# Kernel optimization log

Measured on AMD Instinct MI355X. Metric: run time of the kernel, lower is better.

The kernel has to match this reference:

```python
import jax, jax.numpy as jnp
import numpy as np

WS = 5       # window_size
SHIFT = 2    # shift_size
NH = 3       # num_heads (hardcoded in module)
EPS = 1e-5   # LayerNorm eps (torch default)

B, H, W, C = 4, 400, 400, 48


def _window_partition(x, ws):
    b, h, w, c = x.shape
    x = x.reshape(b, h // ws, ws, w // ws, ws, c).transpose(0, 1, 3, 2, 4, 5)
    return x.reshape(-1, ws * ws, c)  # [B*nH*nW, ws*ws, C]


def _window_reverse(x, ws, h, w):
    bn = x.shape[0] // ((h // ws) * (w // ws))
    x = x.reshape(bn, h // ws, w // ws, ws, ws, -1).transpose(0, 1, 3, 2, 4, 5)
    return x.reshape(bn, h, w, -1)


def _qkv_branch(win, qkv_w, qkv_b, ln_g, ln_b):
    # Linear -> LayerNorm(last dim) -> Softmax over window-position axis (dim 1)
    y = win @ qkv_w + qkv_b                      # [B_, N, 3C]
    mu = jnp.mean(y, axis=-1, keepdims=True)
    var = jnp.mean((y - mu) ** 2, axis=-1, keepdims=True)
    y = (y - mu) * jax.lax.rsqrt(var + EPS) * ln_g + ln_b
    y = jax.nn.softmax(y, axis=1)                # nn.Softmax(1)
    b_, n, _ = y.shape
    y = y.reshape(b_, n, 3, NH, C // NH).transpose(2, 0, 3, 1, 4)  # [3, B_, h, N, d]
    return y[0], y[1], y[2]


def setup_inputs() -> dict:
    key = jax.random.key(0)
    ks = jax.random.split(key, 4)
    lr_patch = jax.random.normal(ks[0], (B, H, W, C), jnp.float32)
    ref_patch = jax.random.normal(ks[1], (B, H, W, C), jnp.float32)
    qkv_w = jax.random.normal(ks[2], (C, 3 * C), jnp.float32) * (1.0 / np.sqrt(C))
    qkv_b = jax.random.normal(ks[3], (3 * C,), jnp.float32) * 0.01
    ln_g = jnp.ones((3 * C,), jnp.float32)
    ln_b = jnp.zeros((3 * C,), jnp.float32)
    return {"lr_patch": lr_patch, "ref_patch": ref_patch, "qkv_w": qkv_w,
            "qkv_b": qkv_b, "ln_g": ln_g, "ln_b": ln_b}


def reference(lr_patch, ref_patch, qkv_w, qkv_b, ln_g, ln_b):
    # cyclic shift
    s_lr = jnp.roll(lr_patch, shift=(-SHIFT, -SHIFT), axis=(1, 2))
    s_ref = jnp.roll(ref_patch, shift=(-SHIFT, -SHIFT), axis=(1, 2))

    lr_w = _window_partition(s_lr, WS)    # [B_, N=25, C]
    ref_w = _window_partition(s_ref, WS)

    q_lr, k_lr, v_lr = _qkv_branch(lr_w, qkv_w, qkv_b, ln_g, ln_b)
    q_ref, k_ref, v_ref = _qkv_branch(ref_w, qkv_w, qkv_b, ln_g, ln_b)

    # dual cross-attention (no scaling / no second softmax, as in source)
    attn1 = jnp.einsum('bhnd,bhmd->bhnm', q_lr, k_ref)   # [B_, h, N, N]
    attn2 = jnp.einsum('bhnd,bhmd->bhnm', q_ref, k_lr)
    x = jnp.einsum('bhnm,bhmd->bhnd', attn1, v_ref)
    x = jnp.einsum('bhnm,bhmd->bhnd', attn2, x)

    b_, _, n, _ = x.shape
    x = x.transpose(0, 2, 1, 3).reshape(b_, n, C)        # [B_, N, C]
    x = x.reshape(-1, WS, WS, C)

    x = _window_reverse(x, WS, H, W)
    x = jnp.roll(x, shift=(SHIFT, SHIFT), axis=(1, 2))
    return (x, ref_patch)
```

## Files before the change

kernel.cpp:

```cpp
#include <hip/hip_runtime.h>
#include <hip/hip_bf16.h>

typedef __hip_bfloat16 hbf16;
typedef unsigned short u16t;
typedef __attribute__((ext_vector_type(8))) short bf16x8;
typedef __attribute__((ext_vector_type(4))) float f32x4;

#define WSZ 5
#define CC 48
#define C3 144
#define HDIM 400
#define NWH 80
#define SH 2
#define ITERS 4
#define YROWS 57
#define YW 152
#define WTW 56
#define PW 40

__device__ __forceinline__ u16t f2b(float x) {
    union { hbf16 h; u16t u; } c;
    c.h = __float2bfloat16(x);
    return c.u;
}
__device__ __forceinline__ unsigned pk2(float lo, float hi) {
    return ((unsigned)f2b(hi) << 16) | f2b(lo);
}
__device__ __forceinline__ float dpp_add16(float x) {
    int t;
    t = __builtin_amdgcn_update_dpp(0, __float_as_int(x), 0xB1, 0xF, 0xF, true);
    x += __int_as_float(t);
    t = __builtin_amdgcn_update_dpp(0, __float_as_int(x), 0x4E, 0xF, 0xF, true);
    x += __int_as_float(t);
    t = __builtin_amdgcn_update_dpp(0, __float_as_int(x), 0x141, 0xF, 0xF, true);
    x += __int_as_float(t);
    t = __builtin_amdgcn_update_dpp(0, __float_as_int(x), 0x140, 0xF, 0xF, true);
    x += __int_as_float(t);
    return x;
}

__global__ __launch_bounds__(512, 4) void swin_mfma7(
    const float* __restrict__ lr, const float* __restrict__ ref,
    const float* __restrict__ qkv_w, const float* __restrict__ qkv_b,
    const float* __restrict__ ln_g, const float* __restrict__ ln_b,
    float* __restrict__ out, float* __restrict__ out1)
{
    __shared__ __align__(16) u16t s_wT[C3 * WTW];
    __shared__ __align__(16) u16t s_y[2][YROWS * YW];
    __shared__ __align__(16) u16t s_P[2][3 * 32 * PW];
    __shared__ __align__(16) u16t s_x1T[2][3 * 16 * PW];
    __shared__ __align__(16) float s_ln[2][4][16][4];
    __shared__ __align__(16) float s_gb[3 * C3];

    const int tid = threadIdx.x;
    const int wave = tid >> 6, lane = tid & 63;
    const int lm = lane & 15, g = lane >> 4;
    const int wh = wave >> 2;
    const int w4 = wave & 3;
    const int br = w4 >> 1, jh = w4 & 1;
    const int T0 = jh ? 4 : 0;
    const bool gok = (g < 2);

    for (int i = tid; i < CC * C3; i += 512) {
        int c = i / C3, j = i % C3;
        s_wT[j * WTW + c] = f2b(qkv_w[i]);
    }
    for (int i = tid; i < C3; i += 512) {
        s_gb[i] = qkv_b[i];
        s_gb[C3 + i] = ln_g[i];
        s_gb[2 * C3 + i] = ln_b[i];
    }
    for (int i = tid; i < 7 * YW; i += 512) {
        s_y[0][25 * YW + i] = 0;
        s_y[1][25 * YW + i] = 0;
    }
    __syncthreads();

    const bf16x8 z8 = {0, 0, 0, 0, 0, 0, 0, 0};
    const f32x4  z4 = {0.f, 0.f, 0.f, 0.f};
    const float* xsrc = br ? ref : lr;

    for (int it = 0; it < ITERS; ++it) {
        const int wid = blockIdx.x * (2 * ITERS) + it * 2 + wh;
        const int bb = wid / (NWH * NWH);
        const int rr = wid % (NWH * NWH);
        const int bh = rr / NWH, bw = rr % NWH;

        bf16x8 xa[2], xb[2];
        #pragma unroll
        for (int s2 = 0; s2 < 2; ++s2) {
            int row = 16 * s2 + lm;
            int wi = row / WSZ, wj = row % WSZ;
            int hh = bh * WSZ + wi + SH; if (hh >= HDIM) hh -= HDIM;
            int ww = bw * WSZ + wj + SH; if (ww >= HDIM) ww -= HDIM;
            const float4* p4 = reinterpret_cast<const float4*>(
                xsrc + ((size_t)(bb * HDIM + hh) * HDIM + ww) * CC);
            float4 u = p4[2 * g], v = p4[2 * g + 1];
            bf16x8 t;
            t[0] = f2b(u.x); t[1] = f2b(u.y); t[2] = f2b(u.z); t[3] = f2b(u.w);
            t[4] = f2b(v.x); t[5] = f2b(v.y); t[6] = f2b(v.z); t[7] = f2b(v.w);
            xa[s2] = t;
            float4 u2, v2;
            if (gok) {
                u2 = p4[8 + 2 * g]; v2 = p4[9 + 2 * g];
                bf16x8 t2;
                t2[0] = f2b(u2.x); t2[1] = f2b(u2.y); t2[2] = f2b(u2.z); t2[3] = f2b(u2.w);
                t2[4] = f2b(v2.x); t2[5] = f2b(v2.y); t2[6] = f2b(v2.z); t2[7] = f2b(v2.w);
                xb[s2] = t2;
            } else xb[s2] = z8;
            if (w4 == 3 && row < 25) {
                float4* o1 = reinterpret_cast<float4*>(
                    out1 + ((size_t)(bb * HDIM + hh) * HDIM + ww) * CC);
                o1[2 * g] = u; o1[2 * g + 1] = v;
                if (gok) { o1[8 + 2 * g] = u2; o1[9 + 2 * g] = v2; }
            }
        }

        f32x4 acc[5][2];
        #pragma unroll
        for (int tt = 0; tt < 5; ++tt) {
            const int t = T0 + tt;
            bf16x8 w1 = *reinterpret_cast<const bf16x8*>(&s_wT[(16 * t + lm) * WTW + 8 * g]);
            bf16x8 w2 = *reinterpret_cast<const bf16x8*>(&s_wT[(16 * t + lm) * WTW + 32 + 8 * (g & 1)]);
            f32x4 bv = *reinterpret_cast<const f32x4*>(&s_gb[16 * t + 4 * g]);
            #pragma unroll
            for (int s2 = 0; s2 < 2; ++s2) {
                f32x4 a = bv;
                a = __builtin_amdgcn_mfma_f32_16x16x32_bf16(w1, xa[s2], a, 0, 0, 0);
                a = __builtin_amdgcn_mfma_f32_16x16x32_bf16(w2, xb[s2], a, 0, 0, 0);
                acc[tt][s2] = a;
            }
        }

        float s0 = 0.f, q0 = 0.f, s1 = 0.f, q1 = 0.f;
        #pragma unroll
        for (int tt = 0; tt < 5; ++tt) {
            if (jh == 0 || tt > 0) {
                #pragma unroll
                for (int r2 = 0; r2 < 4; ++r2) {
                    float va = acc[tt][0][r2]; s0 += va; q0 += va * va;
                    float vb = acc[tt][1][r2]; s1 += vb; q1 += vb * vb;
                }
            }
        }
        s0 += __shfl_xor(s0, 16); s0 += __shfl_xor(s0, 32);
        q0 += __shfl_xor(q0, 16); q0 += __shfl_xor(q0, 32);
        s1 += __shfl_xor(s1, 16); s1 += __shfl_xor(s1, 32);
        q1 += __shfl_xor(q1, 16); q1 += __shfl_xor(q1, 32);
        if (lane < 16) {
            float4 w4v = make_float4(s0, q0, s1, q1);
            *reinterpret_cast<float4*>(&s_ln[wh][w4][lm][0]) = w4v;
        }
        __syncthreads();
        {
            float4 p = *reinterpret_cast<const float4*>(&s_ln[wh][w4 ^ 1][lm][0]);
            float S0 = s0 + p.x, Q0 = q0 + p.y, S1 = s1 + p.z, Q1 = q1 + p.w;
            float mu0 = S0 * (1.f / 144.f);
            float rs0 = rsqrtf(Q0 * (1.f / 144.f) - mu0 * mu0 + 1e-5f);
            float mu1 = S1 * (1.f / 144.f);
            float rs1 = rsqrtf(Q1 * (1.f / 144.f) - mu1 * mu1 + 1e-5f);
            #pragma unroll
            for (int tt = 0; tt < 5; ++tt) {
                const int t = T0 + tt;
                f32x4 gv = *reinterpret_cast<const f32x4*>(&s_gb[C3 + 16 * t + 4 * g]);
                f32x4 bv2 = *reinterpret_cast<const f32x4*>(&s_gb[2 * C3 + 16 * t + 4 * g]);
                #pragma unroll
                for (int r2 = 0; r2 < 4; ++r2) {
                    acc[tt][0][r2] = (acc[tt][0][r2] - mu0) * rs0 * gv[r2] + bv2[r2];
                    acc[tt][1][r2] = (acc[tt][1][r2] - mu1) * rs1 * gv[r2] + bv2[r2];
                }
            }
        }

        #pragma unroll
        for (int tt = 0; tt < 5; ++tt) {
            const int t = T0 + tt;
            float pa[4], pb[4];
            #pragma unroll
            for (int r2 = 0; r2 < 4; ++r2) {
                float va = acc[tt][0][r2];
                float vb = (lm < 9) ? acc[tt][1][r2] : -1e30f;
                float ea = __expf(va), eb = __expf(vb);
                float ss = dpp_add16(ea + eb);
                float inv = __builtin_amdgcn_rcpf(ss);
                pa[r2] = ea * inv; pb[r2] = eb * inv;
            }
            int colw = 16 * t + 4 * g;
            uint2 wv;
            wv.x = pk2(pa[0], pa[1]); wv.y = pk2(pa[2], pa[3]);
            *reinterpret_cast<uint2*>(&s_y[wh][(32 * br + lm) * YW + colw]) = wv;
            if (lm < 9) {
                wv.x = pk2(pb[0], pb[1]); wv.y = pk2(pb[2], pb[3]);
                *reinterpret_cast<uint2*>(&s_y[wh][(32 * br + 16 + lm) * YW + colw]) = wv;
            }
        }
        __syncthreads();

        if (w4 < 3) {
            const int h = w4;
            const int ko = 8 * (g & 1);
            const bool lok = (lm < 9);
            const u16t* Y = s_y[wh];
            u16t* Ph = &s_P[wh][h * 32 * PW];
            u16t* Xh = &s_x1T[wh][h * 16 * PW];
            __builtin_amdgcn_s_setprio(1);
            bf16x8 ka0 = gok ? *reinterpret_cast<const bf16x8*>(&Y[(32 + lm) * YW + CC + 16 * h + ko]) : z8;
            bf16x8 ka1 = (gok && lok) ? *reinterpret_cast<const bf16x8*>(&Y[(48 + lm) * YW + CC + 16 * h + ko]) : z8;
            bf16x8 qb0 = *reinterpret_cast<const bf16x8*>(&Y[lm * YW + 16 * h + ko]);
            bf16x8 qb1 = *reinterpret_cast<const bf16x8*>(&Y[(16 + lm) * YW + 16 * h + ko]);
            f32x4 p00 = __builtin_amdgcn_mfma_f32_16x16x32_bf16(ka0, qb0, z4, 0, 0, 0);
            f32x4 p01 = __builtin_amdgcn_mfma_f32_16x16x32_bf16(ka0, qb1, z4, 0, 0, 0);
            f32x4 p10 = __builtin_amdgcn_mfma_f32_16x16x32_bf16(ka1, qb0, z4, 0, 0, 0);
            f32x4 p11 = __builtin_amdgcn_mfma_f32_16x16x32_bf16(ka1, qb1, z4, 0, 0, 0);
            uint2 wv;
            wv.x = pk2(p00[0], p00[1]); wv.y = pk2(p00[2], p00[3]);
            *reinterpret_cast<uint2*>(&Ph[lm * PW + 4 * g]) = wv;
            wv.x = pk2(p01[0], p01[1]); wv.y = pk2(p01[2], p01[3]);
            *reinterpret_cast<uint2*>(&Ph[(16 + lm) * PW + 4 * g]) = wv;
            wv.x = pk2(p10[0], p10[1]); wv.y = pk2(p10[2], p10[3]);
            *reinterpret_cast<uint2*>(&Ph[lm * PW + 16 + 4 * g]) = wv;
            wv.x = pk2(p11[0], p11[1]); wv.y = pk2(p11[2], p11[3]);
            *reinterpret_cast<uint2*>(&Ph[(16 + lm) * PW + 16 + 4 * g]) = wv;
            bf16x8 vfr;
            #pragma unroll
            for (int j = 0; j < 8; ++j) {
                int m = 8 * g + j;
                vfr[j] = (m < 25) ? (short)Y[(32 + m) * YW + 96 + 16 * h + lm] : (short)0;
            }
            bf16x8 a0 = *reinterpret_cast<const bf16x8*>(&Ph[lm * PW + 8 * g]);
            bf16x8 a1 = *reinterpret_cast<const bf16x8*>(&Ph[(16 + lm) * PW + 8 * g]);
            f32x4 x10 = __builtin_amdgcn_mfma_f32_16x16x32_bf16(a0, vfr, z4, 0, 0, 0);
            f32x4 x11 = __builtin_amdgcn_mfma_f32_16x16x32_bf16(a1, vfr, z4, 0, 0, 0);
            wv.x = pk2(x10[0], x10[1]); wv.y = pk2(x10[2], x10[3]);
            *reinterpret_cast<uint2*>(&Xh[lm * PW + 4 * g]) = wv;
            wv.x = pk2(x11[0], x11[1]); wv.y = pk2(x11[2], x11[3]);
            *reinterpret_cast<uint2*>(&Xh[lm * PW + 16 + 4 * g]) = wv;
            bf16x8 kb0 = gok ? *reinterpret_cast<const bf16x8*>(&Y[lm * YW + CC + 16 * h + ko]) : z8;
            bf16x8 kb1 = gok ? *reinterpret_cast<const bf16x8*>(&Y[(16 + lm) * YW + CC + 16 * h + ko]) : z8;
            bf16x8 qc0 = *reinterpret_cast<const bf16x8*>(&Y[(32 + lm) * YW + 16 * h + ko]);
            bf16x8 qc1 = lok ? *reinterpret_cast<const bf16x8*>(&Y[(48 + lm) * YW + 16 * h + ko]) : z8;
            p00 = __builtin_amdgcn_mfma_f32_16x16x32_bf16(kb0, qc0, z4, 0, 0, 0);
            p01 = __builtin_amdgcn_mfma_f32_16x16x32_bf16(kb0, qc1, z4, 0, 0, 0);
            p10 = __builtin_amdgcn_mfma_f32_16x16x32_bf16(kb1, qc0, z4, 0, 0, 0);
            p11 = __builtin_amdgcn_mfma_f32_16x16x32_bf16(kb1, qc1, z4, 0, 0, 0);
            wv.x = pk2(p00[0], p00[1]); wv.y = pk2(p00[2], p00[3]);
            *reinterpret_cast<uint2*>(&Ph[lm * PW + 4 * g]) = wv;
            wv.x = pk2(p01[0], p01[1]); wv.y = pk2(p01[2], p01[3]);
            *reinterpret_cast<uint2*>(&Ph[(16 + lm) * PW + 4 * g]) = wv;
            wv.x = pk2(p10[0], p10[1]); wv.y = pk2(p10[2], p10[3]);
            *reinterpret_cast<uint2*>(&Ph[lm * PW + 16 + 4 * g]) = wv;
            wv.x = pk2(p11[0], p11[1]); wv.y = pk2(p11[2], p11[3]);
            *reinterpret_cast<uint2*>(&Ph[(16 + lm) * PW + 16 + 4 * g]) = wv;
            bf16x8 xv = *reinterpret_cast<const bf16x8*>(&Xh[lm * PW + 8 * g]);
            bf16x8 pb0 = *reinterpret_cast<const bf16x8*>(&Ph[lm * PW + 8 * g]);
            bf16x8 pb1 = *reinterpret_cast<const bf16x8*>(&Ph[(16 + lm) * PW + 8 * g]);
            f32x4 o0 = __builtin_amdgcn_mfma_f32_16x16x32_bf16(xv, pb0, z4, 0, 0, 0);
            f32x4 o1v = __builtin_amdgcn_mfma_f32_16x16x32_bf16(xv, pb1, z4, 0, 0, 0);
            __builtin_amdgcn_s_setprio(0);
            #pragma unroll
            for (int nt = 0; nt < 2; ++nt) {
                int n2 = 16 * nt + lm;
                if (n2 < 25) {
                    f32x4 ov = nt ? o1v : o0;
                    int wi2 = n2 / WSZ, wj2 = n2 % WSZ;
                    int oh = bh * WSZ + wi2 + SH; if (oh >= HDIM) oh -= HDIM;
                    int ow = bw * WSZ + wj2 + SH; if (ow >= HDIM) ow -= HDIM;
                    float4 o = make_float4(ov[0], ov[1], ov[2], ov[3]);
                    *reinterpret_cast<float4*>(
                        &out[((size_t)(bb * HDIM + oh) * HDIM + ow) * CC + 16 * h + 4 * g]) = o;
                }
            }
        }
    }
}

extern "C" void kernel_launch(void* const* d_in, const int* in_sizes, int n_in,
                              void* d_out, int out_size, void* d_ws, size_t ws_size,
                              hipStream_t stream) {
    const float* lr    = (const float*)d_in[0];
    const float* ref   = (const float*)d_in[1];
    const float* qkv_w = (const float*)d_in[2];
    const float* qkv_b = (const float*)d_in[3];
    const float* ln_g  = (const float*)d_in[4];
    const float* ln_b  = (const float*)d_in[5];
    float* out = (float*)d_out;
    float* out1 = out + (size_t)out_size / 2;

    const int n_blocks = 4 * NWH * NWH / (2 * ITERS);
    swin_mfma7<<<n_blocks, 512, 0, stream>>>(lr, ref, qkv_w, qkv_b, ln_g, ln_b, out, out1);
}
```

Measured before the change: 264.6 us.

## Shrink blocks to one window per iteration and move ref copy to idle wave

Blocks go from 512 threads (two windows per iteration) to 256 threads (one window per iteration). Each block now runs 8 iterations, so the grid keeps the same total window count with the same number of blocks. The out1 copy of ref_patch leaves the load phase and runs on the fourth wave, which is otherwise idle during the attention stage; that wave re-reads ref from global memory. The aim is to cut shared memory per block and barrier scope, raising occupancy, and to overlap the passthrough copy with attention work. The cost is an extra global read of ref and less parallel work per block.

```diff
diff --git a/kernel.cpp b/kernel.cpp
--- a/kernel.cpp
+++ b/kernel.cpp
@@ -12,7 +12,7 @@
 #define HDIM 400
 #define NWH 80
 #define SH 2
-#define ITERS 4
+#define ITERS 8
 #define YROWS 57
 #define YW 152
 #define WTW 56
@@ -39,41 +39,37 @@
     return x;
 }
 
-__global__ __launch_bounds__(512, 4) void swin_mfma7(
+__global__ __launch_bounds__(256, 4) void swin_mfma8(
     const float* __restrict__ lr, const float* __restrict__ ref,
     const float* __restrict__ qkv_w, const float* __restrict__ qkv_b,
     const float* __restrict__ ln_g, const float* __restrict__ ln_b,
     float* __restrict__ out, float* __restrict__ out1)
 {
     __shared__ __align__(16) u16t s_wT[C3 * WTW];
-    __shared__ __align__(16) u16t s_y[2][YROWS * YW];
-    __shared__ __align__(16) u16t s_P[2][3 * 32 * PW];
-    __shared__ __align__(16) u16t s_x1T[2][3 * 16 * PW];
-    __shared__ __align__(16) float s_ln[2][4][16][4];
+    __shared__ __align__(16) u16t s_y[YROWS * YW];
+    __shared__ __align__(16) u16t s_P[3 * 32 * PW];
+    __shared__ __align__(16) u16t s_x1T[3 * 16 * PW];
+    __shared__ __align__(16) float s_ln[4][16][4];
     __shared__ __align__(16) float s_gb[3 * C3];
 
     const int tid = threadIdx.x;
     const int wave = tid >> 6, lane = tid & 63;
     const int lm = lane & 15, g = lane >> 4;
-    const int wh = wave >> 2;
-    const int w4 = wave & 3;
+    const int w4 = wave;
     const int br = w4 >> 1, jh = w4 & 1;
     const int T0 = jh ? 4 : 0;
     const bool gok = (g < 2);
 
-    for (int i = tid; i < CC * C3; i += 512) {
+    for (int i = tid; i < CC * C3; i += 256) {
         int c = i / C3, j = i % C3;
         s_wT[j * WTW + c] = f2b(qkv_w[i]);
     }
-    for (int i = tid; i < C3; i += 512) {
+    for (int i = tid; i < C3; i += 256) {
         s_gb[i] = qkv_b[i];
         s_gb[C3 + i] = ln_g[i];
         s_gb[2 * C3 + i] = ln_b[i];
     }
-    for (int i = tid; i < 7 * YW; i += 512) {
-        s_y[0][25 * YW + i] = 0;
-        s_y[1][25 * YW + i] = 0;
-    }
+    for (int i = tid; i < 7 * YW; i += 256) s_y[25 * YW + i] = 0;
     __syncthreads();
 
     const bf16x8 z8 = {0, 0, 0, 0, 0, 0, 0, 0};
@@ -81,7 +77,7 @@
     const float* xsrc = br ? ref : lr;
 
     for (int it = 0; it < ITERS; ++it) {
-        const int wid = blockIdx.x * (2 * ITERS) + it * 2 + wh;
+        const int wid = blockIdx.x * ITERS + it;
         const int bb = wid / (NWH * NWH);
         const int rr = wid % (NWH * NWH);
         const int bh = rr / NWH, bw = rr % NWH;
@@ -100,20 +96,13 @@
             t[0] = f2b(u.x); t[1] = f2b(u.y); t[2] = f2b(u.z); t[3] = f2b(u.w);
             t[4] = f2b(v.x); t[5] = f2b(v.y); t[6] = f2b(v.z); t[7] = f2b(v.w);
             xa[s2] = t;
-            float4 u2, v2;
             if (gok) {
-                u2 = p4[8 + 2 * g]; v2 = p4[9 + 2 * g];
+                float4 u2 = p4[8 + 2 * g], v2 = p4[9 + 2 * g];
                 bf16x8 t2;
                 t2[0] = f2b(u2.x); t2[1] = f2b(u2.y); t2[2] = f2b(u2.z); t2[3] = f2b(u2.w);
                 t2[4] = f2b(v2.x); t2[5] = f2b(v2.y); t2[6] = f2b(v2.z); t2[7] = f2b(v2.w);
                 xb[s2] = t2;
             } else xb[s2] = z8;
-            if (w4 == 3 && row < 25) {
-                float4* o1 = reinterpret_cast<float4*>(
-                    out1 + ((size_t)(bb * HDIM + hh) * HDIM + ww) * CC);
-                o1[2 * g] = u; o1[2 * g + 1] = v;
-                if (gok) { o1[8 + 2 * g] = u2; o1[9 + 2 * g] = v2; }
-            }
         }
 
         f32x4 acc[5][2];
@@ -149,11 +138,11 @@
         q1 += __shfl_xor(q1, 16); q1 += __shfl_xor(q1, 32);
         if (lane < 16) {
             float4 w4v = make_float4(s0, q0, s1, q1);
-            *reinterpret_cast<float4*>(&s_ln[wh][w4][lm][0]) = w4v;
+            *reinterpret_cast<float4*>(&s_ln[w4][lm][0]) = w4v;
         }
         __syncthreads();
         {
-            float4 p = *reinterpret_cast<const float4*>(&s_ln[wh][w4 ^ 1][lm][0]);
+            float4 p = *reinterpret_cast<const float4*>(&s_ln[w4 ^ 1][lm][0]);
             float S0 = s0 + p.x, Q0 = q0 + p.y, S1 = s1 + p.z, Q1 = q1 + p.w;
             float mu0 = S0 * (1.f / 144.f);
             float rs0 = rsqrtf(Q0 * (1.f / 144.f) - mu0 * mu0 + 1e-5f);
@@ -188,10 +177,10 @@
             int colw = 16 * t + 4 * g;
             uint2 wv;
             wv.x = pk2(pa[0], pa[1]); wv.y = pk2(pa[2], pa[3]);
-            *reinterpret_cast<uint2*>(&s_y[wh][(32 * br + lm) * YW + colw]) = wv;
+            *reinterpret_cast<uint2*>(&s_y[(32 * br + lm) * YW + colw]) = wv;
             if (lm < 9) {
                 wv.x = pk2(pb[0], pb[1]); wv.y = pk2(pb[2], pb[3]);
-                *reinterpret_cast<uint2*>(&s_y[wh][(32 * br + 16 + lm) * YW + colw]) = wv;
+                *reinterpret_cast<uint2*>(&s_y[(32 * br + 16 + lm) * YW + colw]) = wv;
             }
         }
         __syncthreads();
@@ -200,9 +189,9 @@
             const int h = w4;
             const int ko = 8 * (g & 1);
             const bool lok = (lm < 9);
-            const u16t* Y = s_y[wh];
-            u16t* Ph = &s_P[wh][h * 32 * PW];
-            u16t* Xh = &s_x1T[wh][h * 16 * PW];
+            const u16t* Y = s_y;
+            u16t* Ph = &s_P[h * 32 * PW];
+            u16t* Xh = &s_x1T[h * 16 * PW];
             __builtin_amdgcn_s_setprio(1);
             bf16x8 ka0 = gok ? *reinterpret_cast<const bf16x8*>(&Y[(32 + lm) * YW + CC + 16 * h + ko]) : z8;
             bf16x8 ka1 = (gok && lok) ? *reinterpret_cast<const bf16x8*>(&Y[(48 + lm) * YW + CC + 16 * h + ko]) : z8;
@@ -270,6 +259,25 @@
                         &out[((size_t)(bb * HDIM + oh) * HDIM + ow) * CC + 16 * h + 4 * g]) = o;
                 }
             }
+        } else {
+            #pragma unroll
+            for (int s2 = 0; s2 < 2; ++s2) {
+                int row = 16 * s2 + lm;
+                if (row < 25) {
+                    int wi = row / WSZ, wj = row % WSZ;
+                    int hh = bh * WSZ + wi + SH; if (hh >= HDIM) hh -= HDIM;
+                    int ww = bw * WSZ + wj + SH; if (ww >= HDIM) ww -= HDIM;
+                    size_t pix = ((size_t)(bb * HDIM + hh) * HDIM + ww) * CC;
+                    const float4* p4 = reinterpret_cast<const float4*>(ref + pix);
+                    float4* o1 = reinterpret_cast<float4*>(out1 + pix);
+                    o1[2 * g] = p4[2 * g];
+                    o1[2 * g + 1] = p4[2 * g + 1];
+                    if (gok) {
+                        o1[8 + 2 * g] = p4[8 + 2 * g];
+                        o1[9 + 2 * g] = p4[9 + 2 * g];
+                    }
+                }
+            }
         }
     }
 }
@@ -286,6 +294,6 @@
     float* out = (float*)d_out;
     float* out1 = out + (size_t)out_size / 2;
 
-    const int n_blocks = 4 * NWH * NWH / (2 * ITERS);
-    swin_mfma7<<<n_blocks, 512, 0, stream>>>(lr, ref, qkv_w, qkv_b, ln_g, ln_b, out, out1);
-}
+    const int n_blocks = 4 * NWH * NWH / ITERS;
+    swin_mfma8<<<n_blocks, 256, 0, stream>>>(lr, ref, qkv_w, qkv_b, ln_g, ln_b, out, out1);
+}
```

Result: slower. 289.2 us (+9.3%).
